# Kernel optimization log

Measured on AMD Instinct MI355X. Metric: run time of the kernel, lower is better.

Reference implementation:

```python
import jax, jax.numpy as jnp
import numpy as np

NEG = -1000000000.0  # matches torch masked_fill value


def setup_inputs() -> dict:
    key = jax.random.key(0)
    ks = jax.random.split(key, 9)
    B, L, E = 2, 2048, 1024
    s = 0.02
    return {
        "query": jax.random.normal(ks[0], (B, L, E), dtype=jnp.float32),
        "w_q_w": jax.random.normal(ks[1], (E, E), dtype=jnp.float32) * s,
        "w_q_b": jax.random.normal(ks[2], (E,), dtype=jnp.float32) * s,
        "w_k_w": jax.random.normal(ks[3], (E, E), dtype=jnp.float32) * s,
        "w_k_b": jax.random.normal(ks[4], (E,), dtype=jnp.float32) * s,
        "w_v_w": jax.random.normal(ks[5], (E, E), dtype=jnp.float32) * s,
        "w_v_b": jax.random.normal(ks[6], (E,), dtype=jnp.float32) * s,
        "w_o_w": jax.random.normal(ks[7], (E, E), dtype=jnp.float32) * s,
        "w_o_b": jax.random.normal(ks[8], (E,), dtype=jnp.float32) * s,
    }


def reference(query, w_q_w, w_q_b, w_k_w, w_k_b, w_v_w, w_v_b, w_o_w, w_o_b):
    # self-attention: key = value = query (forward passes None for key/value)
    B, L, E = query.shape
    H = 16
    d_k = E // H
    scale = 1.0 / jnp.sqrt(jnp.float32(d_k))

    def proj(x, w, b):
        # torch Linear: x @ w.T + b ; then split heads -> [B, H, L, d_k]
        return (x @ w.T + b).reshape(B, L, H, d_k).transpose(0, 2, 1, 3)

    Q = proj(query, w_q_w, w_q_b)
    K = proj(query, w_k_w, w_k_b)
    V = proj(query, w_v_w, w_v_b)

    # full L x S score matrix, as in the eager original
    scores = jnp.einsum('bhqd,bhkd->bhqk', Q, K) * scale
    # causal attn_bias: upper triangle filled with -1e9 (is_causal=True path)
    causal = jnp.tril(jnp.ones((L, L), dtype=bool))
    scores = scores + jnp.where(causal, 0.0, NEG).astype(scores.dtype)
    # softmax, clear_nan (nan -> 0), + 1e-12 epsilon; dropout_p = 0.0 (no-op)
    attn = jnp.nan_to_num(jax.nn.softmax(scores, axis=-1), nan=0.0) + 1e-12

    ctx = jnp.einsum('bhqk,bhkd->bhqd', attn, V)  # [B,H,L,d_k]
    ctx = ctx.transpose(0, 2, 1, 3).reshape(B, L, E)
    return ctx @ w_o_w.T + w_o_b
```

## Files before the change

kernel.cpp:

```cpp
#include <hip/hip_runtime.h>
#include <hip/hip_bf16.h>
#include <math.h>

typedef __bf16 bf16;
typedef __bf16 bf16x4 __attribute__((ext_vector_type(4)));
typedef __bf16 bf16x8 __attribute__((ext_vector_type(8)));
typedef float  f32x4  __attribute__((ext_vector_type(4)));
typedef float  float4v __attribute__((ext_vector_type(4)));
typedef unsigned short u16x4 __attribute__((ext_vector_type(4)));

#define MFMA(a,b,c) __builtin_amdgcn_mfma_f32_16x16x32_bf16((a),(b),(c),0,0,0)

#define QSCALE 0.18033688011112042f
#define EXP2(x) __builtin_amdgcn_exp2f(x)

__device__ __forceinline__ void gload16(const bf16* g, bf16* l) {
  __builtin_amdgcn_global_load_lds(
      (const __attribute__((address_space(1))) void*)g,
      (__attribute__((address_space(3))) void*)l, 16, 0, 0);
}

__device__ __forceinline__ int detect_f32(const unsigned short* __restrict__ p) {
  int bad = 0;
  #pragma unroll
  for (int j = 0; j < 32; ++j) {
    const float x = __uint_as_float(((unsigned)p[j]) << 16);
    bad |= !(fabsf(x) <= 0.5f);
  }
  return bad;
}

__global__ void cvt_all_kernel(const void* x, const void* wq, const void* wk,
                               const void* wv, const void* wo,
                               const void* bq, const void* bk, const void* bv,
                               const void* bo,
                               bf16* cX, bf16* cWq, bf16* cWk, bf16* cWv,
                               bf16* cWo, bf16* cB)
{
  const int isf = detect_f32((const unsigned short*)bq);
  const int NX = 1048576, NW = 262144, NB = 256;
  const int total = NX + 4 * NW + 4 * NB;
  for (int gid = blockIdx.x * blockDim.x + threadIdx.x; gid < total;
       gid += gridDim.x * blockDim.x) {
    const void* s; bf16* d; int off;
    if (gid < NX)                { s = x;  d = cX;  off = gid; }
    else if (gid < NX + NW)      { s = wq; d = cWq; off = gid - NX; }
    else if (gid < NX + 2 * NW)  { s = wk; d = cWk; off = gid - NX - NW; }
    else if (gid < NX + 3 * NW)  { s = wv; d = cWv; off = gid - NX - 2 * NW; }
    else if (gid < NX + 4 * NW)  { s = wo; d = cWo; off = gid - NX - 3 * NW; }
    else {
      const int r = gid - NX - 4 * NW;
      const int wb = r / NB; off = r % NB;
      s = (wb == 0) ? bq : (wb == 1) ? bk : (wb == 2) ? bv : bo;
      d = cB + wb * 1024;
    }
    float4v v;
    if (isf) v = ((const float4v*)s)[off];
    else {
      u16x4 u = ((const u16x4*)s)[off];
      v = (float4v){__uint_as_float((unsigned)u.x << 16),
                    __uint_as_float((unsigned)u.y << 16),
                    __uint_as_float((unsigned)u.z << 16),
                    __uint_as_float((unsigned)u.w << 16)};
    }
    bf16x4 ov = {(bf16)v.x, (bf16)v.y, (bf16)v.z, (bf16)v.w};
    *(bf16x4*)&d[off * 4] = ov;
  }
}

static __device__ __forceinline__ void gemm128_core(
    const bf16* __restrict__ X, const bf16* __restrict__ W,
    int bm, int bn, f32x4 acc[4][4])
{
  __shared__ __align__(16) bf16 Als[128][64];
  __shared__ __align__(16) bf16 Bls[128][64];
  const int t    = threadIdx.x;
  const int lane = t & 63;
  const int w    = t >> 6;
  const int wr   = w >> 1, wc = w & 1;
  const int fr   = lane & 15;
  const int fq   = lane >> 4;
  const int lrow = lane >> 3;
  const int lcol = (lane & 7) * 8;

  #pragma unroll
  for (int m = 0; m < 4; ++m)
    #pragma unroll
    for (int n = 0; n < 4; ++n)
      acc[m][n] = (f32x4){0.f, 0.f, 0.f, 0.f};

  for (int k0 = 0; k0 < 1024; k0 += 64) {
    __syncthreads();
    #pragma unroll
    for (int p = 0; p < 4; ++p) {
      const int rb = p * 32 + w * 8;
      gload16(&X[(size_t)(bm + rb + lrow) * 1024 + k0 + lcol], &Als[rb][0]);
      gload16(&W[(size_t)(bn + rb + lrow) * 1024 + k0 + lcol], &Bls[rb][0]);
    }
    __syncthreads();
    #pragma unroll
    for (int kk = 0; kk < 64; kk += 32) {
      bf16x8 a[4], b[4];
      #pragma unroll
      for (int m = 0; m < 4; ++m)
        a[m] = *(const bf16x8*)&Als[wr * 64 + m * 16 + fr][kk + fq * 8];
      #pragma unroll
      for (int n = 0; n < 4; ++n)
        b[n] = *(const bf16x8*)&Bls[wc * 64 + n * 16 + fr][kk + fq * 8];
      __builtin_amdgcn_s_setprio(1);
      #pragma unroll
      for (int m = 0; m < 4; ++m)
        #pragma unroll
        for (int n = 0; n < 4; ++n)
          acc[m][n] = MFMA(a[m], b[n], acc[m][n]);
      __builtin_amdgcn_s_setprio(0);
    }
  }
}

__global__ __launch_bounds__(256, 3) void qkv_kernel(
    const bf16* __restrict__ X,
    const bf16* __restrict__ Wq, const bf16* __restrict__ Wk,
    const bf16* __restrict__ Wv, const bf16* __restrict__ Bias,
    bf16* __restrict__ Qo, bf16* __restrict__ Ko, bf16* __restrict__ Vto)
{
  const bf16 *W, *bias;
  bf16 *out;
  const int z = blockIdx.z;
  if (z == 0)      { W = Wq; bias = Bias;        out = Qo;  }
  else if (z == 1) { W = Wk; bias = Bias + 1024; out = Ko;  }
  else             { W = Wv; bias = Bias + 2048; out = Vto; }

  const int bm = blockIdx.x * 128, bn = blockIdx.y * 128;
  f32x4 acc[4][4];
  gemm128_core(X, W, bm, bn, acc);

  const int t = threadIdx.x, lane = t & 63, w = t >> 6;
  const int wr = w >> 1, wc = w & 1;
  const int fr = lane & 15, fq = lane >> 4;
  const float qs = (z == 0) ? QSCALE : 1.0f;

  #pragma unroll
  for (int n = 0; n < 4; ++n) {
    const int col = bn + wc * 64 + n * 16 + fr;
    const float bb = (float)bias[col];
    const int h = col >> 6, d = col & 63;
    if (z != 2) {
      #pragma unroll
      for (int m = 0; m < 4; ++m)
        #pragma unroll
        for (int r = 0; r < 4; ++r) {
          const int row = bm + wr * 64 + m * 16 + fq * 4 + r;
          const int b = row >> 11, li = row & 2047;
          out[(size_t)((b * 16 + h) * 2048 + li) * 64 + d] =
              (bf16)((acc[m][n][r] + bb) * qs);
        }
    } else {
      #pragma unroll
      for (int m = 0; m < 4; ++m) {
        const int tok0 = bm + wr * 64 + m * 16 + fq * 4;
        const int b = tok0 >> 11, li0 = tok0 & 2047;
        bf16x4 pk = {(bf16)(acc[m][n][0] + bb), (bf16)(acc[m][n][1] + bb),
                     (bf16)(acc[m][n][2] + bb), (bf16)(acc[m][n][3] + bb)};
        *(bf16x4*)&out[(size_t)((b * 16 + h) * 64 + d) * 2048 + li0] = pk;
      }
    }
  }
}

__device__ __forceinline__ f32x4 fmax4(f32x4 a, f32x4 b) {
  return (f32x4){fmaxf(a[0], b[0]), fmaxf(a[1], b[1]),
                 fmaxf(a[2], b[2]), fmaxf(a[3], b[3])};
}

__global__ __launch_bounds__(256, 4) void attn_kernel(
    const bf16* __restrict__ Q, const bf16* __restrict__ K,
    const bf16* __restrict__ Vt, bf16* __restrict__ CTX)
{
  const int bx = (int)blockIdx.x;
  const int gen = bx >> 8;
  const int u = bx & 255;
  const int bh = u >> 3;
  const int j = u & 7;
  int qt;
  if (gen == 0)      qt = 31 - j;
  else if (gen == 1) qt = 16 + j;
  else if (gen == 2) qt = 15 - j;
  else               qt = j;

  const int t = threadIdx.x, lane = t & 63, w = t >> 6;
  const int fr = lane & 15, fq = lane >> 4;
  const bf16* Qb = Q  + (size_t)bh * 2048 * 64;
  const bf16* Kb = K  + (size_t)bh * 2048 * 64;
  const bf16* Vb = Vt + (size_t)bh * 64 * 2048;
  const int q0 = qt * 64 + w * 16;
  const int myq = q0 + fr;
  const int nt = qt + 1;

  __shared__ __align__(16) bf16 Kls[2][64][64];
  __shared__ __align__(16) bf16 Vls[2][64][64];
  __shared__ __align__(16) bf16 Pls[4][16][64];

  const int X7   = (fr & 7) << 4;
  const int off0 = fr * 128 + ((fq * 16) ^ X7);
  const int off1 = fr * 128 + ((64 + fq * 16) ^ X7);
  const char* Kb0 = (const char*)Kls;
  const char* Vb0 = (const char*)Vls;
  char* Pw = (char*)Pls + w * 2048 + fr * 128;
  int pwoff[4];
  #pragma unroll
  for (int g = 0; g < 4; ++g) pwoff[g] = ((g * 32 + fq * 8) ^ X7);
  const int proff0 = ((fq * 16) ^ X7);
  const int proff1 = ((64 + fq * 16) ^ X7);

  const int r8 = lane >> 3;
  const int cb = (lane & 7) << 4;
  const int sc = (cb ^ (r8 << 4)) >> 1;
  const bf16* gk0 = Kb + (size_t)(w * 8 + r8) * 64 + sc;
  const bf16* gk1 = Kb + (size_t)(32 + w * 8 + r8) * 64 + sc;
  const bf16* gv0 = Vb + (size_t)(w * 8 + r8) * 2048 + sc;
  const bf16* gv1 = Vb + (size_t)(32 + w * 8 + r8) * 2048 + sc;

  const bf16x8 qf0 = *(const bf16x8*)&Qb[(size_t)(q0 + fr) * 64 + fq * 8];
  const bf16x8 qf1 = *(const bf16x8*)&Qb[(size_t)(q0 + fr) * 64 + 32 + fq * 8];

  f32x4 o[4];
  #pragma unroll
  for (int g = 0; g < 4; ++g) o[g] = (f32x4){0.f, 0.f, 0.f, 0.f};
  float m_r = -1e30f;
  float s_part = 0.f;

  gload16(gk0, &Kls[0][w * 8][0]);
  gload16(gk1, &Kls[0][32 + w * 8][0]);
  gload16(gv0, &Vls[0][w * 8][0]);
  gload16(gv1, &Vls[0][32 + w * 8][0]);
  gk0 += 4096; gk1 += 4096; gv0 += 64; gv1 += 64;
  __syncthreads();
  int cur = 0;

  for (int kt = 0; kt < nt; ++kt) {
    if (kt + 1 < nt) {
      bf16 (*Kn)[64] = Kls[cur ^ 1];
      bf16 (*Vn)[64] = Vls[cur ^ 1];
      gload16(gk0, &Kn[w * 8][0]);
      gload16(gk1, &Kn[32 + w * 8][0]);
      gload16(gv0, &Vn[w * 8][0]);
      gload16(gv1, &Vn[32 + w * 8][0]);
      gk0 += 4096; gk1 += 4096; gv0 += 64; gv1 += 64;
    }

    const char* kb = Kb0 + (cur << 13);
    const char* vb = Vb0 + (cur << 13);

    f32x4 S[4];
    __builtin_amdgcn_s_setprio(1);
    #pragma unroll
    for (int g = 0; g < 4; ++g) {
      bf16x8 kf0 = *(const bf16x8*)(kb + off0 + g * 2048);
      bf16x8 kf1 = *(const bf16x8*)(kb + off1 + g * 2048);
      f32x4 s = (f32x4){0.f, 0.f, 0.f, 0.f};
      s = MFMA(kf0, qf0, s);
      s = MFMA(kf1, qf1, s);
      S[g] = s;
    }
    __builtin_amdgcn_s_setprio(0);

    if (kt == qt) {
      #pragma unroll
      for (int g = 0; g < 4; ++g)
        #pragma unroll
        for (int r = 0; r < 4; ++r)
          S[g][r] = (kt * 64 + g * 16 + fq * 4 + r <= myq) ? S[g][r] : -1e9f;
    }
    f32x4 mv = fmax4(fmax4(S[0], S[1]), fmax4(S[2], S[3]));
    const float mxl = fmaxf(fmaxf(mv[0], mv[1]), fmaxf(mv[2], mv[3]));
    if (!__all(mxl <= m_r + 8.f)) {
      float mxq = fmaxf(mxl, __shfl_xor(mxl, 16));
      mxq = fmaxf(mxq, __shfl_xor(mxq, 32));
      const float mnew = fmaxf(m_r, mxq);
      const float f = EXP2(m_r - mnew);
      m_r = mnew;
      s_part *= f;
      float frow[4];
      #pragma unroll
      for (int r = 0; r < 4; ++r) frow[r] = __shfl(f, fq * 4 + r, 64);
      #pragma unroll
      for (int g = 0; g < 4; ++g)
        #pragma unroll
        for (int r = 0; r < 4; ++r) o[g][r] *= frow[r];
    }
    #pragma unroll
    for (int g = 0; g < 4; ++g)
      #pragma unroll
      for (int r = 0; r < 4; ++r) {
        const float p = EXP2(S[g][r] - m_r);
        S[g][r] = p;
        s_part += p;
      }
    #pragma unroll
    for (int g = 0; g < 4; ++g) {
      bf16x4 pk = {(bf16)S[g][0], (bf16)S[g][1], (bf16)S[g][2], (bf16)S[g][3]};
      *(bf16x4*)(Pw + pwoff[g]) = pk;
    }
    __builtin_amdgcn_s_setprio(1);
    {
      bf16x8 pa0 = *(const bf16x8*)(Pw + proff0);
      #pragma unroll
      for (int g2 = 0; g2 < 4; ++g2) {
        bf16x8 vf = *(const bf16x8*)(vb + off0 + g2 * 2048);
        o[g2] = MFMA(pa0, vf, o[g2]);
      }
      bf16x8 pa1 = *(const bf16x8*)(Pw + proff1);
      #pragma unroll
      for (int g2 = 0; g2 < 4; ++g2) {
        bf16x8 vf = *(const bf16x8*)(vb + off1 + g2 * 2048);
        o[g2] = MFMA(pa1, vf, o[g2]);
      }
    }
    __builtin_amdgcn_s_setprio(0);
    __syncthreads();
    cur ^= 1;
  }

  float s_r = s_part;
  s_r += __shfl_xor(s_r, 16);
  s_r += __shfl_xor(s_r, 32);
  const float inv = __builtin_amdgcn_rcpf(fmaxf(s_r, 1e-30f));
  float invr[4];
  #pragma unroll
  for (int r = 0; r < 4; ++r) invr[r] = __shfl(inv, fq * 4 + r, 64);
  const int b = bh >> 4, h = bh & 15;
  #pragma unroll
  for (int r = 0; r < 4; ++r) {
    const int tok = b * 2048 + q0 + fq * 4 + r;
    #pragma unroll
    for (int g2 = 0; g2 < 4; ++g2)
      CTX[(size_t)tok * 1024 + h * 64 + g2 * 16 + fr] =
          (bf16)(o[g2][r] * invr[r]);
  }
}

__global__ __launch_bounds__(256, 3) void out_kernel(
    const bf16* __restrict__ CTXi, const bf16* __restrict__ Wo,
    const bf16* __restrict__ bo, void* __restrict__ Y,
    const unsigned short* __restrict__ det)
{
  const int isf = detect_f32(det);
  const int bm = blockIdx.x * 128, bn = blockIdx.y * 128;
  f32x4 acc[4][4];
  gemm128_core(CTXi, Wo, bm, bn, acc);

  const int t = threadIdx.x, lane = t & 63, w = t >> 6;
  const int wr = w >> 1, wc = w & 1;
  const int fr = lane & 15, fq = lane >> 4;

  #pragma unroll
  for (int n = 0; n < 4; ++n) {
    const int col = bn + wc * 64 + n * 16 + fr;
    const float bb = (float)bo[col];
    #pragma unroll
    for (int m = 0; m < 4; ++m)
      #pragma unroll
      for (int r = 0; r < 4; ++r) {
        const int row = bm + wr * 64 + m * 16 + fq * 4 + r;
        const size_t idx = (size_t)row * 1024 + col;
        const float v = acc[m][n][r] + bb;
        if (isf) ((float*)Y)[idx] = v;
        else     ((bf16*)Y)[idx] = (bf16)v;
      }
  }
}

extern "C" void kernel_launch(void* const* d_in, const int* in_sizes, int n_in,
                              void* d_out, int out_size, void* d_ws, size_t ws_size,
                              hipStream_t stream) {
  char* ws = (char*)d_ws;
  const size_t MB = 1024 * 1024;

  bf16* cX  = (bf16*)(ws + 1 * MB);
  bf16* cWq = (bf16*)(ws + 9 * MB);
  bf16* cWk = (bf16*)(ws + 11 * MB);
  bf16* cWv = (bf16*)(ws + 13 * MB);
  bf16* cWo = (bf16*)(ws + 15 * MB);
  bf16* cB  = (bf16*)(ws + 17 * MB);
  bf16* Qw  = (bf16*)(ws + 18 * MB);
  bf16* Kw  = (bf16*)(ws + 26 * MB);
  bf16* Vt  = (bf16*)(ws + 34 * MB);
  bf16* CT  = (bf16*)(ws + 42 * MB);

  cvt_all_kernel<<<2048, 256, 0, stream>>>(d_in[0], d_in[1], d_in[3], d_in[5],
                                           d_in[7], d_in[2], d_in[4], d_in[6],
                                           d_in[8], cX, cWq, cWk, cWv, cWo, cB);

  qkv_kernel<<<dim3(32, 8, 3), 256, 0, stream>>>(cX, cWq, cWk, cWv, cB,
                                                 Qw, Kw, Vt);
  attn_kernel<<<1024, 256, 0, stream>>>(Qw, Kw, Vt, CT);
  out_kernel<<<dim3(32, 8), 256, 0, stream>>>(CT, cWo, cB + 3072, d_out,
                                              (const unsigned short*)d_in[2]);
}
```

Baseline: 113.8 us.

## Use 128-row attention tiles with 8 waves; shrink out-projection tiles to 128x64

The attention kernel now runs 512 threads per block, each block covering 128 query rows with 8 waves. The K/V tiles are shared across the waves, halving loads per thread, and waves skip fully masked key tiles. The output projection switches from the shared 128x128 GEMM core to its own 128x64-tile loop, doubling the grid to 512 blocks for better CU fill. The trade-offs are fewer attention blocks (512), waves idling at barriers on skipped tiles, and a simpler unpipelined out-GEMM loop.

```diff
diff --git a/kernel.cpp b/kernel.cpp
--- a/kernel.cpp
+++ b/kernel.cpp
@@ -173,7 +173,7 @@
                  fmaxf(a[2], b[2]), fmaxf(a[3], b[3])};
 }
 
-__global__ __launch_bounds__(256, 4) void attn_kernel(
+__global__ __launch_bounds__(512, 4) void attn_kernel(
     const bf16* __restrict__ Q, const bf16* __restrict__ K,
     const bf16* __restrict__ Vt, bf16* __restrict__ CTX)
 {
@@ -182,24 +182,20 @@
   const int u = bx & 255;
   const int bh = u >> 3;
   const int j = u & 7;
-  int qt;
-  if (gen == 0)      qt = 31 - j;
-  else if (gen == 1) qt = 16 + j;
-  else if (gen == 2) qt = 15 - j;
-  else               qt = j;
+  const int qt = gen ? j : 15 - j;
 
   const int t = threadIdx.x, lane = t & 63, w = t >> 6;
   const int fr = lane & 15, fq = lane >> 4;
   const bf16* Qb = Q  + (size_t)bh * 2048 * 64;
   const bf16* Kb = K  + (size_t)bh * 2048 * 64;
   const bf16* Vb = Vt + (size_t)bh * 64 * 2048;
-  const int q0 = qt * 64 + w * 16;
+  const int q0 = qt * 128 + w * 16;
   const int myq = q0 + fr;
-  const int nt = qt + 1;
+  const int nt = 2 * qt + 2;
 
   __shared__ __align__(16) bf16 Kls[2][64][64];
   __shared__ __align__(16) bf16 Vls[2][64][64];
-  __shared__ __align__(16) bf16 Pls[4][16][64];
+  __shared__ __align__(16) bf16 Pls[8][16][64];
 
   const int X7   = (fr & 7) << 4;
   const int off0 = fr * 128 + ((fq * 16) ^ X7);
@@ -216,10 +212,8 @@
   const int r8 = lane >> 3;
   const int cb = (lane & 7) << 4;
   const int sc = (cb ^ (r8 << 4)) >> 1;
-  const bf16* gk0 = Kb + (size_t)(w * 8 + r8) * 64 + sc;
-  const bf16* gk1 = Kb + (size_t)(32 + w * 8 + r8) * 64 + sc;
-  const bf16* gv0 = Vb + (size_t)(w * 8 + r8) * 2048 + sc;
-  const bf16* gv1 = Vb + (size_t)(32 + w * 8 + r8) * 2048 + sc;
+  const bf16* gk = Kb + (size_t)(w * 8 + r8) * 64 + sc;
+  const bf16* gv = Vb + (size_t)(w * 8 + r8) * 2048 + sc;
 
   const bf16x8 qf0 = *(const bf16x8*)&Qb[(size_t)(q0 + fr) * 64 + fq * 8];
   const bf16x8 qf1 = *(const bf16x8*)&Qb[(size_t)(q0 + fr) * 64 + 32 + fq * 8];
@@ -230,94 +224,92 @@
   float m_r = -1e30f;
   float s_part = 0.f;
 
-  gload16(gk0, &Kls[0][w * 8][0]);
-  gload16(gk1, &Kls[0][32 + w * 8][0]);
-  gload16(gv0, &Vls[0][w * 8][0]);
-  gload16(gv1, &Vls[0][32 + w * 8][0]);
-  gk0 += 4096; gk1 += 4096; gv0 += 64; gv1 += 64;
+  gload16(gk, &Kls[0][w * 8][0]);
+  gload16(gv, &Vls[0][w * 8][0]);
+  gk += 4096; gv += 64;
   __syncthreads();
   int cur = 0;
 
   for (int kt = 0; kt < nt; ++kt) {
     if (kt + 1 < nt) {
-      bf16 (*Kn)[64] = Kls[cur ^ 1];
-      bf16 (*Vn)[64] = Vls[cur ^ 1];
-      gload16(gk0, &Kn[w * 8][0]);
-      gload16(gk1, &Kn[32 + w * 8][0]);
-      gload16(gv0, &Vn[w * 8][0]);
-      gload16(gv1, &Vn[32 + w * 8][0]);
-      gk0 += 4096; gk1 += 4096; gv0 += 64; gv1 += 64;
-    }
-
-    const char* kb = Kb0 + (cur << 13);
-    const char* vb = Vb0 + (cur << 13);
-
-    f32x4 S[4];
-    __builtin_amdgcn_s_setprio(1);
-    #pragma unroll
-    for (int g = 0; g < 4; ++g) {
-      bf16x8 kf0 = *(const bf16x8*)(kb + off0 + g * 2048);
-      bf16x8 kf1 = *(const bf16x8*)(kb + off1 + g * 2048);
-      f32x4 s = (f32x4){0.f, 0.f, 0.f, 0.f};
-      s = MFMA(kf0, qf0, s);
-      s = MFMA(kf1, qf1, s);
-      S[g] = s;
-    }
-    __builtin_amdgcn_s_setprio(0);
-
-    if (kt == qt) {
+      gload16(gk, &Kls[cur ^ 1][w * 8][0]);
+      gload16(gv, &Vls[cur ^ 1][w * 8][0]);
+      gk += 4096; gv += 64;
+    }
+
+    const int kbase = kt * 64;
+    if (kbase <= q0 + 15) {
+      const char* kb = Kb0 + (cur << 13);
+      const char* vb = Vb0 + (cur << 13);
+
+      f32x4 S[4];
+      __builtin_amdgcn_s_setprio(1);
+      #pragma unroll
+      for (int g = 0; g < 4; ++g) {
+        bf16x8 kf0 = *(const bf16x8*)(kb + off0 + g * 2048);
+        bf16x8 kf1 = *(const bf16x8*)(kb + off1 + g * 2048);
+        f32x4 s = (f32x4){0.f, 0.f, 0.f, 0.f};
+        s = MFMA(kf0, qf0, s);
+        s = MFMA(kf1, qf1, s);
+        S[g] = s;
+      }
+      __builtin_amdgcn_s_setprio(0);
+
+      if (kbase + 63 > q0) {
+        #pragma unroll
+        for (int g = 0; g < 4; ++g)
+          #pragma unroll
+          for (int r = 0; r < 4; ++r)
+            S[g][r] = (kbase + g * 16 + fq * 4 + r <= myq) ? S[g][r] : -1e9f;
+      }
+      f32x4 mv = fmax4(fmax4(S[0], S[1]), fmax4(S[2], S[3]));
+      const float mxl = fmaxf(fmaxf(mv[0], mv[1]), fmaxf(mv[2], mv[3]));
+      if (!__all(mxl <= m_r + 8.f)) {
+        float mxq = fmaxf(mxl, __shfl_xor(mxl, 16));
+        mxq = fmaxf(mxq, __shfl_xor(mxq, 32));
+        const float mnew = fmaxf(m_r, mxq);
+        const float f = EXP2(m_r - mnew);
+        m_r = mnew;
+        s_part *= f;
+        float frow[4];
+        #pragma unroll
+        for (int r = 0; r < 4; ++r) frow[r] = __shfl(f, fq * 4 + r, 64);
+        #pragma unroll
+        for (int g = 0; g < 4; ++g)
+          #pragma unroll
+          for (int r = 0; r < 4; ++r) o[g][r] *= frow[r];
+      }
       #pragma unroll
       for (int g = 0; g < 4; ++g)
         #pragma unroll
-        for (int r = 0; r < 4; ++r)
-          S[g][r] = (kt * 64 + g * 16 + fq * 4 + r <= myq) ? S[g][r] : -1e9f;
-    }
-    f32x4 mv = fmax4(fmax4(S[0], S[1]), fmax4(S[2], S[3]));
-    const float mxl = fmaxf(fmaxf(mv[0], mv[1]), fmaxf(mv[2], mv[3]));
-    if (!__all(mxl <= m_r + 8.f)) {
-      float mxq = fmaxf(mxl, __shfl_xor(mxl, 16));
-      mxq = fmaxf(mxq, __shfl_xor(mxq, 32));
-      const float mnew = fmaxf(m_r, mxq);
-      const float f = EXP2(m_r - mnew);
-      m_r = mnew;
-      s_part *= f;
-      float frow[4];
-      #pragma unroll
-      for (int r = 0; r < 4; ++r) frow[r] = __shfl(f, fq * 4 + r, 64);
-      #pragma unroll
-      for (int g = 0; g < 4; ++g)
-        #pragma unroll
-        for (int r = 0; r < 4; ++r) o[g][r] *= frow[r];
-    }
-    #pragma unroll
-    for (int g = 0; g < 4; ++g)
-      #pragma unroll
-      for (int r = 0; r < 4; ++r) {
-        const float p = EXP2(S[g][r] - m_r);
-        S[g][r] = p;
-        s_part += p;
-      }
-    #pragma unroll
-    for (int g = 0; g < 4; ++g) {
-      bf16x4 pk = {(bf16)S[g][0], (bf16)S[g][1], (bf16)S[g][2], (bf16)S[g][3]};
-      *(bf16x4*)(Pw + pwoff[g]) = pk;
-    }
-    __builtin_amdgcn_s_setprio(1);
-    {
-      bf16x8 pa0 = *(const bf16x8*)(Pw + proff0);
-      #pragma unroll
-      for (int g2 = 0; g2 < 4; ++g2) {
-        bf16x8 vf = *(const bf16x8*)(vb + off0 + g2 * 2048);
-        o[g2] = MFMA(pa0, vf, o[g2]);
-      }
-      bf16x8 pa1 = *(const bf16x8*)(Pw + proff1);
-      #pragma unroll
-      for (int g2 = 0; g2 < 4; ++g2) {
-        bf16x8 vf = *(const bf16x8*)(vb + off1 + g2 * 2048);
-        o[g2] = MFMA(pa1, vf, o[g2]);
-      }
-    }
-    __builtin_amdgcn_s_setprio(0);
+        for (int r = 0; r < 4; ++r) {
+          const float p = EXP2(S[g][r] - m_r);
+          S[g][r] = p;
+          s_part += p;
+        }
+      #pragma unroll
+      for (int g = 0; g < 4; ++g) {
+        bf16x4 pk = {(bf16)S[g][0], (bf16)S[g][1], (bf16)S[g][2],
+                     (bf16)S[g][3]};
+        *(bf16x4*)(Pw + pwoff[g]) = pk;
+      }
+      __builtin_amdgcn_s_setprio(1);
+      {
+        bf16x8 pa0 = *(const bf16x8*)(Pw + proff0);
+        #pragma unroll
+        for (int g2 = 0; g2 < 4; ++g2) {
+          bf16x8 vf = *(const bf16x8*)(vb + off0 + g2 * 2048);
+          o[g2] = MFMA(pa0, vf, o[g2]);
+        }
+        bf16x8 pa1 = *(const bf16x8*)(Pw + proff1);
+        #pragma unroll
+        for (int g2 = 0; g2 < 4; ++g2) {
+          bf16x8 vf = *(const bf16x8*)(vb + off1 + g2 * 2048);
+          o[g2] = MFMA(pa1, vf, o[g2]);
+        }
+      }
+      __builtin_amdgcn_s_setprio(0);
+    }
     __syncthreads();
     cur ^= 1;
   }
@@ -340,23 +332,63 @@
   }
 }
 
-__global__ __launch_bounds__(256, 3) void out_kernel(
+__global__ __launch_bounds__(256, 4) void out_kernel(
     const bf16* __restrict__ CTXi, const bf16* __restrict__ Wo,
     const bf16* __restrict__ bo, void* __restrict__ Y,
     const unsigned short* __restrict__ det)
 {
+  __shared__ __align__(16) bf16 Als[128][64];
+  __shared__ __align__(16) bf16 Bls[64][64];
   const int isf = detect_f32(det);
-  const int bm = blockIdx.x * 128, bn = blockIdx.y * 128;
-  f32x4 acc[4][4];
-  gemm128_core(CTXi, Wo, bm, bn, acc);
-
+  const int bm = blockIdx.x * 128, bn = blockIdx.y * 64;
   const int t = threadIdx.x, lane = t & 63, w = t >> 6;
   const int wr = w >> 1, wc = w & 1;
   const int fr = lane & 15, fq = lane >> 4;
-
-  #pragma unroll
-  for (int n = 0; n < 4; ++n) {
-    const int col = bn + wc * 64 + n * 16 + fr;
+  const int lrow = lane >> 3;
+  const int lcol = (lane & 7) * 8;
+
+  f32x4 acc[4][2];
+  #pragma unroll
+  for (int m = 0; m < 4; ++m)
+    #pragma unroll
+    for (int n = 0; n < 2; ++n)
+      acc[m][n] = (f32x4){0.f, 0.f, 0.f, 0.f};
+
+  for (int k0 = 0; k0 < 1024; k0 += 64) {
+    __syncthreads();
+    #pragma unroll
+    for (int p = 0; p < 4; ++p) {
+      const int rb = p * 32 + w * 8;
+      gload16(&CTXi[(size_t)(bm + rb + lrow) * 1024 + k0 + lcol], &Als[rb][0]);
+    }
+    #pragma unroll
+    for (int p = 0; p < 2; ++p) {
+      const int rb = w * 16 + p * 8;
+      gload16(&Wo[(size_t)(bn + rb + lrow) * 1024 + k0 + lcol], &Bls[rb][0]);
+    }
+    __syncthreads();
+    #pragma unroll
+    for (int kk = 0; kk < 64; kk += 32) {
+      bf16x8 a[4], b[2];
+      #pragma unroll
+      for (int m = 0; m < 4; ++m)
+        a[m] = *(const bf16x8*)&Als[wr * 64 + m * 16 + fr][kk + fq * 8];
+      #pragma unroll
+      for (int n = 0; n < 2; ++n)
+        b[n] = *(const bf16x8*)&Bls[wc * 32 + n * 16 + fr][kk + fq * 8];
+      __builtin_amdgcn_s_setprio(1);
+      #pragma unroll
+      for (int m = 0; m < 4; ++m)
+        #pragma unroll
+        for (int n = 0; n < 2; ++n)
+          acc[m][n] = MFMA(a[m], b[n], acc[m][n]);
+      __builtin_amdgcn_s_setprio(0);
+    }
+  }
+
+  #pragma unroll
+  for (int n = 0; n < 2; ++n) {
+    const int col = bn + wc * 32 + n * 16 + fr;
     const float bb = (float)bo[col];
     #pragma unroll
     for (int m = 0; m < 4; ++m)
@@ -394,7 +426,7 @@
 
   qkv_kernel<<<dim3(32, 8, 3), 256, 0, stream>>>(cX, cWq, cWk, cWv, cB,
                                                  Qw, Kw, Vt);
-  attn_kernel<<<1024, 256, 0, stream>>>(Qw, Kw, Vt, CT);
-  out_kernel<<<dim3(32, 8), 256, 0, stream>>>(CT, cWo, cB + 3072, d_out,
-                                              (const unsigned short*)d_in[2]);
-}
+  attn_kernel<<<512, 512, 0, stream>>>(Qw, Kw, Vt, CT);
+  out_kernel<<<dim3(32, 16), 256, 0, stream>>>(CT, cWo, cB + 3072, d_out,
+                                               (const unsigned short*)d_in[2]);
+}
```

After: 111.6 us. About the same (-1.9%).
